# Performance work log

Hardware: AMD Instinct MI355X
Metric: run time of the kernel (lower is better)

## Reference

```python
import jax, jax.numpy as jnp
import numpy as np

B = 1; D = 28; H = 28; W = 28; DIM = 192; HEADS = 6
WS = (7, 7, 7); SS = (3, 3, 3)
CH = DIM // HEADS
N = WS[0] * WS[1] * WS[2]
ND, NH, NWW = D // WS[0], H // WS[1], W // WS[2]
NW = ND * NH * NWW
L = D * H * W
HID = 4 * DIM


def _rel_pos_index():
    c = np.stack(np.meshgrid(np.arange(WS[0]), np.arange(WS[1]), np.arange(WS[2]), indexing='ij')).reshape(3, -1)
    r = (c[:, :, None] - c[:, None, :]).transpose(1, 2, 0)
    r[:, :, 0] += WS[0] - 1; r[:, :, 1] += WS[1] - 1; r[:, :, 2] += WS[2] - 1
    r[:, :, 0] *= (2 * WS[1] - 1) * (2 * WS[2] - 1)
    r[:, :, 1] *= 2 * WS[2] - 1
    return r.sum(-1).reshape(-1)

RPI = _rel_pos_index()  # (N*N,)


def _attn_mask():
    img = np.zeros((D, H, W), np.float32)
    cnt = 0
    sl = lambda w, s: (slice(0, -w), slice(-w, -s), slice(-s, None))
    for a in sl(WS[0], SS[0]):
        for bb in sl(WS[1], SS[1]):
            for cc in sl(WS[2], SS[2]):
                img[a, bb, cc] = cnt; cnt += 1
    mw = img.reshape(ND, WS[0], NH, WS[1], NWW, WS[2]).transpose(0, 2, 4, 1, 3, 5).reshape(-1, N)
    return np.where(mw[:, None, :] != mw[:, :, None], np.float32(-100.0), np.float32(0.0))

MASK = jnp.asarray(_attn_mask())  # (NW, N, N)


def ln(x, g, b):
    mu = x.mean(-1, keepdims=True)
    v = ((x - mu) ** 2).mean(-1, keepdims=True)
    return (x - mu) * jax.lax.rsqrt(v + 1e-5) * g + b


def conv3d(x, w, pad):
    return jax.lax.conv_general_dilated(x, w, (1, 1, 1), [(pad, pad)] * 3,
                                        dimension_numbers=('NCDHW', 'OIDHW', 'NCDHW'))


def bn3d(x, g, b):
    mu = x.mean((0, 2, 3, 4), keepdims=True)
    var = x.var((0, 2, 3, 4), keepdims=True)
    return (x - mu) * jax.lax.rsqrt(var + 1e-5) * g.reshape(1, -1, 1, 1, 1) + b.reshape(1, -1, 1, 1, 1)


def offset_block(x, w1, g1, b1, w2, g2, b2, w3):
    x = jax.nn.relu(bn3d(conv3d(x, w1, 1), g1, b1))
    x = jax.nn.relu(bn3d(conv3d(x, w2, 1), g2, b2))
    return conv3d(x, w3, 0)  # (B, 3*HEADS, D, H, W)


def warp(vol, flow):
    # vol: (B,HEADS,CH,D,H,W), flow: (B,HEADS,3,D,H,W) voxel displacements; trilinear, border-clamped
    gd, gh, gw = jnp.meshgrid(jnp.arange(D, dtype=jnp.float32), jnp.arange(H, dtype=jnp.float32),
                              jnp.arange(W, dtype=jnp.float32), indexing='ij')
    cd = jnp.clip(gd + flow[:, :, 0], 0.0, D - 1)
    chh = jnp.clip(gh + flow[:, :, 1], 0.0, H - 1)
    cw = jnp.clip(gw + flow[:, :, 2], 0.0, W - 1)
    d0 = jnp.floor(cd).astype(jnp.int32); d1 = jnp.minimum(d0 + 1, D - 1)
    h0 = jnp.floor(chh).astype(jnp.int32); h1 = jnp.minimum(h0 + 1, H - 1)
    w0 = jnp.floor(cw).astype(jnp.int32); w1 = jnp.minimum(w0 + 1, W - 1)
    fd = (cd - d0).reshape(B, HEADS, 1, -1)
    fh = (chh - h0).reshape(B, HEADS, 1, -1)
    fw = (cw - w0).reshape(B, HEADS, 1, -1)
    vf = vol.reshape(B, HEADS, CH, -1)
    def gat(di, hi, wi):
        idx = ((di * H + hi) * W + wi).reshape(B, HEADS, 1, -1)
        return jnp.take_along_axis(vf, idx, axis=3)
    out = (gat(d0, h0, w0) * (1 - fd) * (1 - fh) * (1 - fw)
           + gat(d0, h0, w1) * (1 - fd) * (1 - fh) * fw
           + gat(d0, h1, w0) * (1 - fd) * fh * (1 - fw)
           + gat(d0, h1, w1) * (1 - fd) * fh * fw
           + gat(d1, h0, w0) * fd * (1 - fh) * (1 - fw)
           + gat(d1, h0, w1) * fd * (1 - fh) * fw
           + gat(d1, h1, w0) * fd * fh * (1 - fw)
           + gat(d1, h1, w1) * fd * fh * fw)
    return out.reshape(B, HEADS, CH, D, H, W)


def win_part(x):  # (B,D,H,W,C) -> (B*NW, N, C)
    c = x.shape[-1]
    x = x.reshape(B, ND, WS[0], NH, WS[1], NWW, WS[2], c)
    return x.transpose(0, 1, 3, 5, 2, 4, 6, 7).reshape(B * NW, N, c)


def dwin_part(x):  # (B,HEADS,D,H,W,CH) -> (B*NW, N, DIM)
    x = x.reshape(B, HEADS, ND, WS[0], NH, WS[1], NWW, WS[2], CH)
    x = x.transpose(0, 2, 4, 6, 3, 5, 7, 1, 8)
    return x.reshape(B * NW, N, DIM)


def win_rev(x):  # (B*NW, N, DIM) -> (B,D,H,W,DIM)
    x = x.reshape(B, ND, NH, NWW, WS[0], WS[1], WS[2], DIM)
    return x.transpose(0, 1, 4, 2, 5, 3, 6, 7).reshape(B, D, H, W, DIM)


def kv(x, w, b):
    y = (x @ w.T + b).reshape(x.shape[0], N, 2, HEADS, CH).transpose(2, 0, 3, 1, 4)
    return y[0], y[1]


def to_heads(x):
    return x.reshape(x.shape[0], N, HEADS, CH).transpose(0, 2, 1, 3)


def _forward(mov, fix, norm1_g, norm1_b, offm_w1, offm_g1, offm_b1, offm_w2, offm_g2, offm_b2, offm_w3, offf_w1, offf_g1, offf_b1, offf_w2, offf_g2, offf_b2, offf_w3, mq_w, mq_b, mkv_w, mkv_b, fq_w, fq_b, fkv_w, fkv_b, mproj_w, mproj_b, fproj_w, fproj_b, rpb_table, norm2_g, norm2_b, fc1_w, fc1_b, fc2_w, fc2_b):
    m = ln(mov, norm1_g, norm1_b).reshape(B, D, H, W, DIM)
    f = ln(fix, norm1_g, norm1_b).reshape(B, D, H, W, DIM)
    off_m = offset_block(jnp.concatenate([m, f], -1).transpose(0, 4, 1, 2, 3), offm_w1, offm_g1, offm_b1, offm_w2, offm_g2, offm_b2, offm_w3)
    off_f = offset_block(jnp.concatenate([f, m], -1).transpose(0, 4, 1, 2, 3), offf_w1, offf_g1, offf_b1, offf_w2, offf_g2, offf_b2, offf_w3)
    mh = m.transpose(0, 4, 1, 2, 3).reshape(B, HEADS, CH, D, H, W)
    fh = f.transpose(0, 4, 1, 2, 3).reshape(B, HEADS, CH, D, H, W)
    dmov = warp(mh, off_m.reshape(B, HEADS, 3, D, H, W)).transpose(0, 1, 3, 4, 5, 2)  # (B,h,D,H,W,c)
    dfix = warp(fh, off_f.reshape(B, HEADS, 3, D, H, W)).transpose(0, 1, 3, 4, 5, 2)
    sh = (-SS[0], -SS[1], -SS[2])
    mw_ = win_part(jnp.roll(m, sh, (1, 2, 3)))
    fw_ = win_part(jnp.roll(f, sh, (1, 2, 3)))
    dmw = dwin_part(jnp.roll(dmov, sh, (2, 3, 4)))
    dfw = dwin_part(jnp.roll(dfix, sh, (2, 3, 4)))
    B_ = B * NW
    scale = CH ** -0.5
    mK, mV = kv(mw_, mkv_w, mkv_b)
    fK, fV = kv(fw_, fkv_w, fkv_b)
    dmQ = to_heads(dmw @ mq_w.T + mq_b) * scale
    dfQ = to_heads(dfw @ fq_w.T + fq_b) * scale
    rpb = rpb_table[RPI].reshape(N, N, HEADS).transpose(2, 0, 1)  # (HEADS,N,N)
    def attend(q, k, v):
        a = jnp.einsum('bhnc,bhmc->bhnm', q, k) + rpb[None]
        a = (a.reshape(B, NW, HEADS, N, N) + MASK[None, :, None]).reshape(B_, HEADS, N, N)
        a = jax.nn.softmax(a, axis=-1)
        return jnp.einsum('bhnm,bhmc->bhnc', a, v).transpose(0, 2, 1, 3).reshape(B_, N, DIM)
    mo = attend(dfQ, mK, mV) @ mproj_w.T + mproj_b
    fo = attend(dmQ, fK, fV) @ fproj_w.T + fproj_b
    mo = jnp.roll(win_rev(mo), SS, (1, 2, 3)).reshape(B, L, DIM)
    fo = jnp.roll(win_rev(fo), SS, (1, 2, 3)).reshape(B, L, DIM)
    m_out = mov + mo
    f_out = fix + fo
    def mlp(x):
        return jax.nn.gelu(x @ fc1_w.T + fc1_b, approximate=False) @ fc2_w.T + fc2_b
    m_out = m_out + mlp(ln(m_out, norm2_g, norm2_b))
    f_out = f_out + mlp(ln(f_out, norm2_g, norm2_b))
    return jnp.stack([m_out, f_out])  # (2, B, L, DIM)


def setup_inputs():
    key = jax.random.key(0)
    ks = iter(jax.random.split(key, 64))
    nrm = lambda shape, s=0.02: jax.random.normal(next(ks), shape, jnp.float32) * s
    d = {}
    d['mov'] = jax.random.normal(next(ks), (B, L, DIM), jnp.float32)
    d['fix'] = jax.random.normal(next(ks), (B, L, DIM), jnp.float32)
    d['norm1_g'] = jnp.ones((DIM,)); d['norm1_b'] = jnp.zeros((DIM,))
    for p in ('offm', 'offf'):
        d[p + '_w1'] = nrm((DIM, 2 * DIM, 3, 3, 3))
        d[p + '_g1'] = jnp.ones((DIM,)); d[p + '_b1'] = jnp.zeros((DIM,))
        d[p + '_w2'] = nrm((DIM // 2, DIM, 3, 3, 3))
        d[p + '_g2'] = jnp.ones((DIM // 2,)); d[p + '_b2'] = jnp.zeros((DIM // 2,))
        d[p + '_w3'] = nrm((3 * HEADS, DIM // 2, 1, 1, 1))
    for p, o in (('mq_w', DIM), ('mkv_w', 2 * DIM), ('fq_w', DIM), ('fkv_w', 2 * DIM), ('mproj_w', DIM), ('fproj_w', DIM)):
        d[p] = nrm((o, DIM))
    for p, o in (('mq_b', DIM), ('mkv_b', 2 * DIM), ('fq_b', DIM), ('fkv_b', 2 * DIM), ('mproj_b', DIM), ('fproj_b', DIM)):
        d[p] = jnp.zeros((o,))
    d['rpb_table'] = nrm(((2 * WS[0] - 1) * (2 * WS[1] - 1) * (2 * WS[2] - 1), HEADS))
    d['norm2_g'] = jnp.ones((DIM,)); d['norm2_b'] = jnp.zeros((DIM,))
    d['fc1_w'] = nrm((HID, DIM)); d['fc1_b'] = jnp.zeros((HID,))
    d['fc2_w'] = nrm((DIM, HID)); d['fc2_b'] = jnp.zeros((DIM,))
    return d


def reference(mov, fix, norm1_g, norm1_b, offm_w1, offm_g1, offm_b1, offm_w2, offm_g2, offm_b2, offm_w3, offf_w1, offf_g1, offf_b1, offf_w2, offf_g2, offf_b2, offf_w3, mq_w, mq_b, mkv_w, mkv_b, fq_w, fq_b, fkv_w, fkv_b, mproj_w, mproj_b, fproj_w, fproj_b, rpb_table, norm2_g, norm2_b, fc1_w, fc1_b, fc2_w, fc2_b):
    return _forward(mov, fix, norm1_g, norm1_b, offm_w1, offm_g1, offm_b1, offm_w2, offm_g2, offm_b2, offm_w3, offf_w1, offf_g1, offf_b1, offf_w2, offf_g2, offf_b2, offf_w3, mq_w, mq_b, mkv_w, mkv_b, fq_w, fq_b, fkv_w, fkv_b, mproj_w, mproj_b, fproj_w, fproj_b, rpb_table, norm2_g, norm2_b, fc1_w, fc1_b, fc2_w, fc2_b)
```

## Files before the change

kernel.cpp:

```cpp
#include <hip/hip_runtime.h>

#define LTOT 21952
#define NTOK 343

typedef unsigned short u16;
typedef unsigned int   u32;
typedef __attribute__((ext_vector_type(8))) short short8;
typedef __attribute__((ext_vector_type(4))) float float4v;

__device__ __forceinline__ u16 f2b(float f){
  u32 x = __float_as_uint(f);
  u32 r = (x + 0x7fffu + ((x>>16)&1u)) >> 16;
  return (u16)r;
}

__device__ __forceinline__ void dma16(const u16* g, u16* l){
  __builtin_amdgcn_global_load_lds((const __attribute__((address_space(1))) u32*)g,
                                   (__attribute__((address_space(3))) u32*)l,
                                   16, 0, 0);
}

__global__ __launch_bounds__(64) void k_ln(const float* __restrict__ mov, const float* __restrict__ fix,
                                           const float* __restrict__ g, const float* __restrict__ b,
                                           float* __restrict__ om, float* __restrict__ of){
// ... 19 lines not shown
  int row = blockIdx.x;
  const float* src = x + (size_t)row*192;
  float* dst = y + (size_t)row*192;
  int t = threadIdx.x;
  float x0 = src[t], x1 = src[t+64], x2 = src[t+128];
  float s = x0+x1+x2, s2 = x0*x0 + x1*x1 + x2*x2;
  for (int o=32;o;o>>=1){ s += __shfl_xor(s,o); s2 += __shfl_xor(s2,o); }
  float mu = s*(1.f/192.f);
  float var = s2*(1.f/192.f) - mu*mu;
  float rs = rsqrtf(var + 1e-5f);
  dst[t]     = (x0-mu)*rs*g[t]     + b[t];
  dst[t+64]  = (x1-mu)*rs*g[t+64]  + b[t+64];
  dst[t+128] = (x2-mu)*rs*g[t+128] + b[t+128];
}

__global__ void k_prepw1b(const float* __restrict__ src, u16* __restrict__ dst, int swap){
  int idx = blockIdx.x*256 + threadIdx.x;
  if (idx >= 192*10368) return;
  int c8 = idx & 7;
  int t2 = idx >> 3;
  int n  = t2 % 192;
  int sw = t2 / 192;
  int k  = (sw>>2)*32 + (sw&3)*8 + c8;
  int t  = k / 384; int c = k - t*384;
  int cs = c + swap; if (cs >= 384) cs -= 384;
  dst[idx] = f2b(src[((size_t)n*384 + cs)*27 + t]);
}
__global__ void k_prepw2b(const float* __restrict__ src, u16* __restrict__ dst){
  int idx = blockIdx.x*256 + threadIdx.x;
  if (idx >= 96*5184) return;
  int n = idx / 5184; int k = idx - n*5184;
  int t = k / 192; int c = k - t*192;
  dst[idx] = f2b(src[((size_t)n*192 + c)*27 + t]);
}
__global__ void k_prepwb(const float* __restrict__ src, u16* __restrict__ dst, int count){
  int idx = blockIdx.x*256 + threadIdx.x;
  if (idx < count) dst[idx] = f2b(src[idx]);
}

__global__ void k_prepbias(const float* __restrict__ rpt, float* __restrict__ bm){
  int idx = blockIdx.x*256 + threadIdx.x;
  if (idx >= 48*123904) return;
  int th = idx / 123904; int r = idx - th*123904;
  int key = r / 352; int q = r - key*352;
  int type = th / 6; int h = th - type*6;
  float v;
  if (key >= 343 || q >= 343){
    v = -30000.f;
  } else {
    int ki = key/49, kj = (key/7)%7, kk = key%7;
    int qi = q/49,   qj = (q/7)%7,   qk = q%7;
    int ridx = ((qi-ki+6)*13 + (qj-kj+6))*13 + (qk-kk+6);
// ... 8 lines not shown

__global__ __launch_bounds__(192) void k_pad1(const float* __restrict__ m_, const float* __restrict__ f_,
                                              u16* __restrict__ xp){
  int p = blockIdx.x; int t = threadIdx.x;
  int pd = p/900; int r = p - pd*900; int ph = r/30; int pw = r - ph*30;
  int d = pd-1, h = ph-1, w = pw-1;
  u16 vm = 0, vf = 0;
  if ((unsigned)d < 28u && (unsigned)h < 28u && (unsigned)w < 28u){
    size_t l = (size_t)((d*28+h)*28+w)*192 + t;
    vm = f2b(m_[l]); vf = f2b(f_[l]);
  }
  xp[(size_t)p*384 + t] = vm;
  xp[(size_t)p*384 + 192 + t] = vf;
}
__global__ __launch_bounds__(192) void k_pad2(const float* __restrict__ t1,
                                              const float* __restrict__ a1, const float* __restrict__ b1,
                                              u16* __restrict__ xp2){
  int p = blockIdx.x; int t = threadIdx.x;
  int pd = p/900; int r = p - pd*900; int ph = r/30; int pw = r - ph*30;
  int d = pd-1, h = ph-1, w = pw-1;
  u16 v = 0;
  if ((unsigned)d < 28u && (unsigned)h < 28u && (unsigned)w < 28u){
    float xv = t1[(size_t)((d*28+h)*28+w)*192 + t];
    v = f2b(fmaxf(xv*a1[t] + b1[t], 0.f));
  }
  xp2[(size_t)p*192 + t] = v;
}

__global__ __launch_bounds__(256, 4) void k_conv1dma(const u16* __restrict__ xp,
                                                     const u16* __restrict__ wmT,
                                                     const u16* __restrict__ wfT,
                                                     float* __restrict__ outm,
                                                     float* __restrict__ outf){
  __shared__ __align__(16) u16 As[2][64*40];
  __shared__ __align__(16) u16 Bs[2][4*1544];
  int tid = threadIdx.x;
  int b0 = blockIdx.x;
  int xcd = b0 & 7, ii = b0 >> 3;
  int bid = (xcd < 6 ? xcd*86 : 516 + (xcd-6)*85) + ii;
  int half = (bid >= 343) ? 1 : 0;
  int t = bid - half*343;
  const u16* wtb = half ? wfT : wmT;
  float* out = half ? outf : outm;
  int v0 = t*64;
  int sv  = tid>>2;
  int c8u = (tid&3)*8;
  int av = v0 + sv;
  int d = av/784; int rm2 = av - d*784; int hh = rm2/28; int ww = rm2 - hh*28;
  int pbase = (d*30 + hh)*30 + ww;
  int lane = tid&63, wv = tid>>6;
// ... 11 lines not shown
    int tp = s/12, cc = s - tp*12;
    int td = tp/9, tr = tp - td*9, th = tr/3, tw = tr - th*3;
    int toff = td*900 + th*30 + tw;
    a_r = *(const uint4*)(xp + (size_t)(pbase + toff)*384 + cc*32 + c8u);
  };
  auto dmaB = [&](int buf, int s){
    const u16* bsrc = wtb + ((size_t)(s*4 + wv)*192)*8 + (size_t)lane*8;
    #pragma unroll
    for (int j=0;j<3;j++)
      dma16(bsrc + j*512, &Bs[buf][wv*1544 + j*512]);
  };
  auto writeA = [&](int buf){
    *(uint4*)(&As[buf][sv*40 + c8u]) = a_r;
  };

  loadA(0);
  dmaB(0, 0);
  writeA(0);
  __syncthreads();
  for (int s = 0; s < 324; s++){
    if (s+1 < 324){ loadA(s+1); dmaB((s+1)&1, s+1); }
    int buf = s&1;
    short8 aa[4], bb[3];
    #pragma unroll
    for (int mt=0; mt<4; mt++)
      aa[mt] = *(const short8*)(&As[buf][(mt*16 + lm)*40 + lq*8]);
    #pragma unroll
    for (int nt=0; nt<3; nt++)
      bb[nt] = *(const short8*)(&Bs[buf][lq*1544 + (nbase + nt*16 + lm)*8]);
    #pragma unroll
    for (int nt=0; nt<3; nt++)
      #pragma unroll
      for (int mt=0; mt<4; mt++)
        acc[mt][nt] = __builtin_amdgcn_mfma_f32_16x16x32_bf16(aa[mt], bb[nt], acc[mt][nt], 0, 0, 0);
    if (s+1 < 324) writeA((s+1)&1);
    __syncthreads();
  }
  #pragma unroll
  for (int mt=0; mt<4; mt++)
    #pragma unroll
    for (int nt=0; nt<3; nt++)
      #pragma unroll
      for (int r=0; r<4; r++){
        int row = v0 + mt*16 + lq*4 + r;
        int col = nbase + nt*16 + lm;
        out[(size_t)row*192 + col] = acc[mt][nt][r];
      }
}

template<int CIN, int COUT>
__global__ __launch_bounds__(256, 4) void k_convmfma(const u16* __restrict__ xpA,
// ... 80 lines not shown
    if (s+1 < STEPS) write_s((s+1)&1);
    __syncthreads();
  }
  #pragma unroll
  for (int mt=0; mt<2; mt++)
    #pragma unroll
    for (int nt=0; nt<NT; nt++)
      #pragma unroll
      for (int r=0; r<4; r++){
        int row = v0 + mbase + mt*16 + lq*4 + r;
        int col = nbase + nt*16 + lm;
        out[(size_t)row*COUT + col] = acc[mt][nt][r];
      }
}

template<int K, int NF, int GATHER, int ASRC, int EPI>
__global__ __launch_bounds__(256) void k_gemm(const float* __restrict__ Af,
                                              const u16* __restrict__ Ab,
                                              const u16* __restrict__ B,
                                              const float* __restrict__ bias,
                                              const float* __restrict__ resid,
                                              float* __restrict__ outf,
                                              u16* __restrict__ out16,
                                              u16* __restrict__ out16b,
                                              float scale){
  constexpr int STEPS = K/32;
  constexpr int NB = NF/64;
  __shared__ __align__(16) u16 As[2][64*40];
  __shared__ __align__(16) u16 Bs[2][64*40];
  __shared__ int map[64];
  int tid = threadIdx.x;
  int bid = blockIdx.x;
  int mb = bid / NB, nb = bid - mb*NB;
  int v0 = mb*64, ncol0 = nb*64;
  if (tid < 64){
    int r = v0 + tid;
    int src;
    if (GATHER == 0){
      src = r;
    } else if (GATHER == 1){
      int w = r/343; int n = r - w*343;
      int nd = w>>4, nh = (w>>2)&3, nw = w&3;
      int i = n/49; int rr = n - i*49; int j = rr/7; int k2 = rr - j*7;
      int dd = nd*7 + i + 3; if (dd >= 28) dd -= 28;
      int hh = nh*7 + j + 3; if (hh >= 28) hh -= 28;
      int ww = nw*7 + k2 + 3; if (ww >= 28) ww -= 28;
      src = (dd*28 + hh)*28 + ww;
    } else {
      int l = r;
      int d = l/784; int rm = l - d*784; int y = rm/28; int x = rm - y*28;
      int dp = d-3; if (dp<0) dp+=28;
      int yp = y-3; if (yp<0) yp+=28;
      int xq = x-3; if (xq<0) xq+=28;
      int nd = dp/7, i = dp - nd*7;
      int nh = yp/7, j = yp - nh*7;
      int nw = xq/7, k2 = xq - nw*7;
      src = ((nd*4+nh)*4+nw)*NTOK + (i*7+j)*7 + k2;
    }
    map[tid] = src;
  }
  __syncthreads();
  int sv = tid>>2, c8 = (tid&3)*8;
  int arow = map[sv];
  int lane = tid&63, wv = tid>>6;
  int lm = lane&15, lq = lane>>4;
  int mbase = (wv>>1)*32, nbase = (wv&1)*32;

  float4v acc[2][2];
  #pragma unroll
  for (int mt=0; mt<2; mt++)
    #pragma unroll
    for (int nt=0; nt<2; nt++) acc[mt][nt] = (float4v)0.f;

  float4 afr0, afr1; uint4 abr; uint4 bvr;
  auto load_s = [&](int s){
    if (ASRC == 0){
      const float* ap = Af + (size_t)arow*K + s*32 + c8;
      afr0 = *(const float4*)ap;
      afr1 = *(const float4*)(ap+4);
    } else {
      abr = *(const uint4*)(Ab + (size_t)arow*K + s*32 + c8);
    }
    bvr = *(const uint4*)(B + (size_t)(ncol0 + sv)*K + s*32 + c8);
  };
  auto write_s = [&](int buf){
    if (ASRC == 0){
      uint4 pk;
      pk.x = (u32)f2b(afr0.x) | ((u32)f2b(afr0.y)<<16);
      pk.y = (u32)f2b(afr0.z) | ((u32)f2b(afr0.w)<<16);
      pk.z = (u32)f2b(afr1.x) | ((u32)f2b(afr1.y)<<16);
      pk.w = (u32)f2b(afr1.z) | ((u32)f2b(afr1.w)<<16);
      *(uint4*)(&As[buf][sv*40 + c8]) = pk;
    } else {
      *(uint4*)(&As[buf][sv*40 + c8]) = abr;
    }
    *(uint4*)(&Bs[buf][sv*40 + c8]) = bvr;
  };

// ... 8 lines not shown
    for (int mt=0; mt<2; mt++)
      aa[mt] = *(const short8*)(&As[buf][(mbase + mt*16 + lm)*40 + lq*8]);
    #pragma unroll
    for (int nt=0; nt<2; nt++)
      bb[nt] = *(const short8*)(&Bs[buf][(nbase + nt*16 + lm)*40 + lq*8]);
    #pragma unroll
    for (int nt=0; nt<2; nt++)
      #pragma unroll
      for (int mt=0; mt<2; mt++)
        acc[mt][nt] = __builtin_amdgcn_mfma_f32_16x16x32_bf16(aa[mt], bb[nt], acc[mt][nt], 0, 0, 0);
    if (s+1 < STEPS) write_s((s+1)&1);
    __syncthreads();
  }
  float bv[2];
  #pragma unroll
  for (int nt=0; nt<2; nt++) bv[nt] = bias ? bias[ncol0 + nbase + nt*16 + lm] : 0.f;
  #pragma unroll
  for (int mt=0; mt<2; mt++){
    #pragma unroll
    for (int r=0; r<4; r++){
      int row = v0 + mbase + mt*16 + lq*4 + r;
      if (EPI == 0 || EPI == 3){
        int w = row/343; int tok = row - w*343;
        #pragma unroll
        for (int nt=0; nt<2; nt++){
          int col = ncol0 + nbase + nt*16 + lm;
          float val = (acc[mt][nt][r] + bv[nt]) * scale;
          if (EPI == 0){
            int h = col>>5, c = col&31;
            out16[((size_t)(w*6 + h)*343 + tok)*32 + c] = f2b(val);
          } else {
            u16* dst = (col < 192) ? out16 : out16b;
            int cc = (col < 192) ? col : col - 192;
            int h = cc>>5, c = cc&31;
            dst[((size_t)(w*6 + h)*343 + tok)*32 + c] = f2b(val);
          }
        }
      } else if (EPI == 1){
        #pragma unroll
        for (int nt=0; nt<2; nt++){
          int col = ncol0 + nbase + nt*16 + lm;
          size_t o = (size_t)row*NF + col;
          outf[o] = acc[mt][nt][r] + bv[nt] + resid[o];
        }
      } else {
        #pragma unroll
        for (int nt=0; nt<2; nt++){
          int col = ncol0 + nbase + nt*16 + lm;
          float v = acc[mt][nt][r] + bv[nt];
          float gl = 0.5f*v*(1.f + erff(v*0.70710678118f));
          out16[(size_t)row*NF + col] = f2b(gl);
        }
      }
    }
  }
}

__global__ __launch_bounds__(192) void k_bnsum(const float* __restrict__ x, int C,
                                               float* __restrict__ psum){
  int bid = blockIdx.x, t = threadIdx.x;
  int rpi = 192/C;
  int c  = (C==192) ? t : (t % 96);
  int ro = (C==192) ? 0 : (t / 96);
  float s=0.f, s2=0.f;
  int base = bid*343;
  for (int r = ro; r < 343; r += rpi){
    float v = x[(size_t)(base+r)*C + c];
    s += v; s2 += v*v;
  }
  psum[(size_t)bid*384 + t]       = s;
  psum[(size_t)bid*384 + 192 + t] = s2;
}
__global__ void k_bnfin(const float* __restrict__ psum, int C,
                        const float* __restrict__ g, const float* __restrict__ b,
                        float* __restrict__ a_out, float* __restrict__ b_out){
  int c = threadIdx.x;
  if (c >= C) return;
  int slots = 192/C;
  float s=0.f, s2=0.f;
  for (int bb=0; bb<64; bb++)
    for (int k=0; k<slots; k++){
      s  += psum[(size_t)bb*384 + k*C + c];
      s2 += psum[(size_t)bb*384 + 192 + k*C + c];
    }
  float mu = s/(float)LTOT;
  float var = s2/(float)LTOT - mu*mu;
  float rstd = rsqrtf(var + 1e-5f);
  float aa = rstd * g[c];
  a_out[c] = aa;
  b_out[c] = b[c] - mu*aa;
}

__global__ __launch_bounds__(96) void k_flow(const float* __restrict__ t2,
                                             const float* __restrict__ a2, const float* __restrict__ b2,
                                             const float* __restrict__ w3, float* __restrict__ flow){
  __shared__ float xr[96];
  int l = blockIdx.x; int t = threadIdx.x;
  float xv = t2[(size_t)l*96 + t];
  xr[t] = fmaxf(xv*a2[t] + b2[t], 0.f);
  __syncthreads();
  if (t < 18){
    float acc = 0.f;
    for (int c=0;c<96;c++) acc += xr[c]*w3[t*96 + c];
    flow[(size_t)t*LTOT + l] = acc;
  }
}

__global__ __launch_bounds__(192) void k_warp(const float* __restrict__ src,
                                              const float* __restrict__ flow, float* __restrict__ dst){
  int l = blockIdx.x; int tid = threadIdx.x; int hh = tid>>5;
  int d = l/784; int rm = l - d*784; int y = rm/28; int x = rm - y*28;
  float fd = flow[(size_t)(hh*3+0)*LTOT + l];
  float fy = flow[(size_t)(hh*3+1)*LTOT + l];
  float fx = flow[(size_t)(hh*3+2)*LTOT + l];
  float cd = fminf(fmaxf((float)d + fd, 0.f), 27.f);
  float cy = fminf(fmaxf((float)y + fy, 0.f), 27.f);
  float cx = fminf(fmaxf((float)x + fx, 0.f), 27.f);
  int d0 = (int)floorf(cd); int d1 = min(d0+1, 27);
  int y0 = (int)floorf(cy); int y1 = min(y0+1, 27);
  int x0 = (int)floorf(cx); int x1 = min(x0+1, 27);
  float wd = cd - (float)d0, wy = cy - (float)y0, wx = cx - (float)x0;
  #define SMP(di,yi,xi) src[(size_t)(((di)*28+(yi))*28+(xi))*192 + tid]
  float v000 = SMP(d0,y0,x0), v001 = SMP(d0,y0,x1), v010 = SMP(d0,y1,x0), v011 = SMP(d0,y1,x1);
  float v100 = SMP(d1,y0,x0), v101 = SMP(d1,y0,x1), v110 = SMP(d1,y1,x0), v111 = SMP(d1,y1,x1);
  #undef SMP
  float o = v000*(1-wd)*(1-wy)*(1-wx) + v001*(1-wd)*(1-wy)*wx
          + v010*(1-wd)*wy*(1-wx)     + v011*(1-wd)*wy*wx
          + v100*wd*(1-wy)*(1-wx)     + v101*wd*(1-wy)*wx
          + v110*wd*wy*(1-wx)         + v111*wd*wy*wx;
  dst[(size_t)l*192 + tid] = o;
}

__global__ __launch_bounds__(256) void k_attmfma(const u16* __restrict__ Q,
                                                 const u16* __restrict__ K,
                                                 const u16* __restrict__ V,
                                                 const float* __restrict__ bm,
                                                 float* __restrict__ ctx){
  __shared__ __align__(16) u16 Kl[352*40];
  __shared__ __align__(16) u16 Vt[32*360];
  __shared__ __align__(16) u16 Pl[4][2][16*40];
  int bid = blockIdx.x;
  int wh = bid/6, qg = bid - (bid/6)*6;
  int w = wh/6, h = wh - w*6;
  int tid = threadIdx.x;
  int nd = w>>4, nh = (w>>2)&3, nw = w&3;
  int type = ((nd==3)?4:0) | ((nh==3)?2:0) | ((nw==3)?1:0);
  const u16* kb = K + (size_t)wh*10976;
  const u16* vbp = V + (size_t)wh*10976;
  for (int idx=tid; idx<343*4; idx+=256){
    int row = idx>>2, c8 = (idx&3)*8;
    uint4 val = *(const uint4*)(kb + row*32 + c8);
    *(uint4*)(&Kl[row*40 + c8]) = val;
  }
  for (int idx=tid; idx<9*40; idx+=256) Kl[343*40 + idx] = 0;
  for (int idx=tid; idx<343*4; idx+=256){
    int row = idx>>2, c8 = (idx&3)*8;
// ... 40 lines not shown
      #pragma unroll
      for (int r=0; r<4; r++){
        float p = __expf(sc[kt][r] - mx);
        sc[kt][r] = p;
        sm += p;
      }
    }
    sm += __shfl_xor(sm, 16);
    sm += __shfl_xor(sm, 32);
    float inv = 1.f/sm;
    float4v o0 = (float4v)0.f, o1 = (float4v)0.f;
    #pragma unroll
    for (int s=0; s<11; s++){
      u16* pw = &Pl[wv][s&1][0];
      #pragma unroll
      for (int half=0; half<2; half++){
        int kt = 2*s + half;
        uint2 pv2;
        pv2.x = (u32)f2b(sc[kt][0]) | ((u32)f2b(sc[kt][1])<<16);
        pv2.y = (u32)f2b(sc[kt][2]) | ((u32)f2b(sc[kt][3])<<16);
        *(uint2*)(&pw[lm*40 + half*16 + lq*4]) = pv2;
      }
      short8 bp = *(const short8*)(&pw[lm*40 + lq*8]);
      short8 a0 = *(const short8*)(&Vt[lm*360 + s*32 + lq*8]);
      short8 a1 = *(const short8*)(&Vt[(16+lm)*360 + s*32 + lq*8]);
      o0 = __builtin_amdgcn_mfma_f32_16x16x32_bf16(a0, bp, o0, 0, 0, 0);
      o1 = __builtin_amdgcn_mfma_f32_16x16x32_bf16(a1, bp, o1, 0, 0, 0);
    }
    int query = q0 + lm;
    if (query < 343){
      float* ob = ctx + ((size_t)w*NTOK + query)*192 + h*32;
      float4 t0, t1v;
      t0.x = o0[0]*inv; t0.y = o0[1]*inv; t0.z = o0[2]*inv; t0.w = o0[3]*inv;
      t1v.x = o1[0]*inv; t1v.y = o1[1]*inv; t1v.z = o1[2]*inv; t1v.w = o1[3]*inv;
      *(float4*)(ob + lq*4) = t0;
      *(float4*)(ob + 16 + lq*4) = t1v;
// ... 35 lines not shown
  const float* mproj_b = (const float*)d_in[28];
  const float* fproj_b = (const float*)d_in[29];
  const float* rpbt    = (const float*)d_in[30];
  const float* n2g     = (const float*)d_in[31];
  const float* n2b     = (const float*)d_in[32];
  const float* fc1_w   = (const float*)d_in[33];
  const float* fc1_b   = (const float*)d_in[34];
  const float* fc2_w   = (const float*)d_in[35];
  const float* fc2_b   = (const float*)d_in[36];
  float* outp = (float*)d_out;

  float* W = (float*)d_ws;
  const size_t L192 = (size_t)LTOT*192;
  float* m_   = W;
  float* f_   = W + 1*L192;
  float* t1m  = W + 2*L192;
  float* t1f  = W + 3*L192;
  u16* xp     = (u16*)(W + 4*L192);
  u16* xp2m   = xp + (size_t)27000*384;
  u16* xp2f   = (u16*)(W + 6*L192);
  float* sb   = W + 6*L192 + 3000000;
  float* a1m = sb,       *b1m = sb+192;
  float* a1f = sb+384,   *b1f = sb+576;
  float* a2m = sb+768,   *b2m = sb+864;
  float* a2f = sb+960,   *b2f = sb+1056;
  float* psum = sb + 1152;
  float* flowm = W + 6*L192 + 3100000;
  float* flowf = flowm + (size_t)LTOT*18;
  float* t2m  = W + 7*L192;
  float* t2f  = W + 7*L192 + (size_t)LTOT*96;
  u16* wt1m = (u16*)(W + 8*L192);
  u16* wt1f = wt1m + 192*10368;
  u16* wt2m = wt1f + 192*10368;
  u16* wt2f = wt2m + 96*5184;
  float* dmov = W + 4*L192;
  float* dfix = W + 5*L192;
  float* ctxm = dmov; float* ctxf = dfix;
  float* mout = m_;   float* fout = f_;
  u16* QMb = (u16*)(W + 6*L192);
  u16* QFb = (u16*)(W + 7*L192);
  u16* Kmb = (u16*)(W + 2*L192);
  u16* Vmb = (u16*)(W + 3*L192);
  u16* Kfb = (u16*)(W + 8*L192);
  u16* Vfb = (u16*)(W + 9*L192);
  float* bm = W;
  u16* wq_m  = (u16*)(W + 9*L192) + 4214784;
  u16* wq_f  = wq_m  + 36864;
  u16* wkv_m = wq_f  + 36864;
  u16* wkv_f = wkv_m + 73728;
  u16* wpj_m = wkv_f + 73728;
  u16* wpj_f = wpj_m + 36864;
  u16* wfc1  = wpj_f + 36864;
  u16* wfc2  = wfc1  + 147456;
  u16* hs16  = (u16*)(W + 2*L192);
  float* lnbuf = W + 6*L192;

  k_prepw1b<<<(192*10368+255)/256, 256, 0, stream>>>(offm_w1, wt1m, 0);
  k_prepw1b<<<(192*10368+255)/256, 256, 0, stream>>>(offf_w1, wt1f, 192);
  k_prepw2b<<<(96*5184+255)/256, 256, 0, stream>>>(offm_w2, wt2m);
  k_prepw2b<<<(96*5184+255)/256, 256, 0, stream>>>(offf_w2, wt2f);
  k_prepwb<<<144, 256, 0, stream>>>(mq_w,    wq_m,  36864);
  k_prepwb<<<144, 256, 0, stream>>>(fq_w,    wq_f,  36864);
  k_prepwb<<<288, 256, 0, stream>>>(mkv_w,   wkv_m, 73728);
  k_prepwb<<<288, 256, 0, stream>>>(fkv_w,   wkv_f, 73728);
  k_prepwb<<<144, 256, 0, stream>>>(mproj_w, wpj_m, 36864);
  k_prepwb<<<144, 256, 0, stream>>>(fproj_w, wpj_f, 36864);
  k_prepwb<<<576, 256, 0, stream>>>(fc1_w,   wfc1,  147456);
  k_prepwb<<<576, 256, 0, stream>>>(fc2_w,   wfc2,  147456);
  k_ln<<<2*LTOT, 64, 0, stream>>>(mov, fix, n1g, n1b, m_, f_);
  k_pad1<<<27000, 192, 0, stream>>>(m_, f_, xp);
  k_conv1dma<<<686, 256, 0, stream>>>(xp, wt1m, wt1f, t1m, t1f);
  k_bnsum<<<64, 192, 0, stream>>>(t1m, 192, psum);
  k_bnfin<<<1, 192, 0, stream>>>(psum, 192, offm_g1, offm_b1, a1m, b1m);
  k_bnsum<<<64, 192, 0, stream>>>(t1f, 192, psum);
  k_bnfin<<<1, 192, 0, stream>>>(psum, 192, offf_g1, offf_b1, a1f, b1f);
  k_pad2<<<27000, 192, 0, stream>>>(t1m, a1m, b1m, xp2m);
  k_pad2<<<27000, 192, 0, stream>>>(t1f, a1f, b1f, xp2f);
  k_convmfma<192,96><<<686, 256, 0, stream>>>(xp2m, xp2f, wt2m, wt2f, t2m, t2f);
  k_bnsum<<<64, 192, 0, stream>>>(t2m, 96, psum);
  k_bnfin<<<1, 96, 0, stream>>>(psum, 96, offm_g2, offm_b2, a2m, b2m);
  k_bnsum<<<64, 192, 0, stream>>>(t2f, 96, psum);
  k_bnfin<<<1, 96, 0, stream>>>(psum, 96, offf_g2, offf_b2, a2f, b2f);
  k_flow<<<LTOT, 96, 0, stream>>>(t2m, a2m, b2m, offm_w3, flowm);
  k_flow<<<LTOT, 96, 0, stream>>>(t2f, a2f, b2f, offf_w3, flowf);
  k_warp<<<LTOT, 192, 0, stream>>>(m_, flowm, dmov);
  k_warp<<<LTOT, 192, 0, stream>>>(f_, flowf, dfix);
  const float scale = 0.17677669529663687f;
  k_gemm<192,192,1,0,0><<<343*3, 256, 0, stream>>>(dmov, nullptr, wq_m,  mq_b,  nullptr, nullptr, QMb, nullptr, scale);
  k_gemm<192,192,1,0,0><<<343*3, 256, 0, stream>>>(dfix, nullptr, wq_f,  fq_b,  nullptr, nullptr, QFb, nullptr, scale);
  k_gemm<192,384,1,0,3><<<343*6, 256, 0, stream>>>(m_,   nullptr, wkv_m, mkv_b, nullptr, nullptr, Kmb, Vmb, 1.f);
  k_gemm<192,384,1,0,3><<<343*6, 256, 0, stream>>>(f_,   nullptr, wkv_f, fkv_b, nullptr, nullptr, Kfb, Vfb, 1.f);
  k_prepbias<<<(48*123904+255)/256, 256, 0, stream>>>(rpbt, bm);
  k_attmfma<<<2304, 256, 0, stream>>>(QFb, Kmb, Vmb, bm, ctxm);
  k_attmfma<<<2304, 256, 0, stream>>>(QMb, Kfb, Vfb, bm, ctxf);
  k_gemm<192,192,2,0,1><<<343*3, 256, 0, stream>>>(ctxm, nullptr, wpj_m, mproj_b, mov, mout, nullptr, nullptr, 1.f);
  k_gemm<192,192,2,0,1><<<343*3, 256, 0, stream>>>(ctxf, nullptr, wpj_f, fproj_b, fix, fout, nullptr, nullptr, 1.f);
  k_ln1<<<LTOT, 64, 0, stream>>>(mout, n2g, n2b, lnbuf);
  k_gemm<192,768,0,0,2><<<343*12, 256, 0, stream>>>(lnbuf, nullptr, wfc1, fc1_b, nullptr, nullptr, hs16, nullptr, 1.f);
  k_gemm<768,192,0,1,1><<<343*3, 256, 0, stream>>>(nullptr, hs16, wfc2, fc2_b, mout, outp, nullptr, nullptr, 1.f);
  k_ln1<<<LTOT, 64, 0, stream>>>(fout, n2g, n2b, lnbuf);
  k_gemm<192,768,0,0,2><<<343*12, 256, 0, stream>>>(lnbuf, nullptr, wfc1, fc1_b, nullptr, nullptr, hs16, nullptr, 1.f);
  k_gemm<768,192,0,1,1><<<343*3, 256, 0, stream>>>(nullptr, hs16, wfc2, fc2_b, fout, outp + L192, nullptr, nullptr, 1.f);
}
```

Before: 1.435 ms.

## Merge moving/fixed kernel launches into batched kernels and triple-buffer conv1

Combines the paired moving/fixed launches (weight prep, BN stats/finalize, pad2, flow, warp, Q/KV/proj GEMMs, attention, LN2 and MLP) into single launches with doubled grids. Per-half pointers are selected from the block index, and contiguous buffers are relied on for the merged LN/MLP path. Separately, conv1 gets a 3-stage LDS pipeline with explicit waitcnt and raw barriers, which lowers its occupancy hint from 4 to 3. The aim is to cut launch count, fill the GPU better in small kernels, and hide load latency in conv1. The cost is more buffer-layout assumptions, e.g. mout/fout and flow halves must be adjacent.

```diff
diff --git a/kernel.cpp b/kernel.cpp
--- a/kernel.cpp
+++ b/kernel.cpp
@@ -57,28 +57,48 @@
   dst[t+128] = (x2-mu)*rs*g[t+128] + b[t+128];
 }
 
-__global__ void k_prepw1b(const float* __restrict__ src, u16* __restrict__ dst, int swap){
+__global__ void k_prepw1b(const float* __restrict__ sm, const float* __restrict__ sf,
+                          u16* __restrict__ dm, u16* __restrict__ df){
   int idx = blockIdx.x*256 + threadIdx.x;
-  if (idx >= 192*10368) return;
-  int c8 = idx & 7;
-  int t2 = idx >> 3;
+  if (idx >= 2*192*10368) return;
+  int half = idx >= 192*10368;
+  int i = idx - half*192*10368;
+  const float* src = half ? sf : sm;
+  u16* dst = half ? df : dm;
+  int swap = half ? 192 : 0;
+  int c8 = i & 7;
+  int t2 = i >> 3;
   int n  = t2 % 192;
   int sw = t2 / 192;
   int k  = (sw>>2)*32 + (sw&3)*8 + c8;
   int t  = k / 384; int c = k - t*384;
   int cs = c + swap; if (cs >= 384) cs -= 384;
-  dst[idx] = f2b(src[((size_t)n*384 + cs)*27 + t]);
-}
-__global__ void k_prepw2b(const float* __restrict__ src, u16* __restrict__ dst){
+  dst[i] = f2b(src[((size_t)n*384 + cs)*27 + t]);
+}
+__global__ void k_prepw2b(const float* __restrict__ sm, const float* __restrict__ sf,
+                          u16* __restrict__ dm, u16* __restrict__ df){
   int idx = blockIdx.x*256 + threadIdx.x;
-  if (idx >= 96*5184) return;
-  int n = idx / 5184; int k = idx - n*5184;
+  if (idx >= 2*96*5184) return;
+  int half = idx >= 96*5184;
+  int i = idx - half*96*5184;
+  const float* src = half ? sf : sm;
+  u16* dst = half ? df : dm;
+  int n = i / 5184; int k = i - n*5184;
   int t = k / 192; int c = k - t*192;
-  dst[idx] = f2b(src[((size_t)n*192 + c)*27 + t]);
-}
-__global__ void k_prepwb(const float* __restrict__ src, u16* __restrict__ dst, int count){
+  dst[i] = f2b(src[((size_t)n*192 + c)*27 + t]);
+}
+__global__ void k_prepwb8(const float* s0,const float* s1,const float* s2,const float* s3,
+                          const float* s4,const float* s5,const float* s6,const float* s7,
+                          u16* d0,u16* d1,u16* d2,u16* d3,u16* d4,u16* d5,u16* d6,u16* d7){
   int idx = blockIdx.x*256 + threadIdx.x;
-  if (idx < count) dst[idx] = f2b(src[idx]);
+  if      (idx < 36864)  d0[idx]        = f2b(s0[idx]);
+  else if (idx < 73728)  d1[idx-36864]  = f2b(s1[idx-36864]);
+  else if (idx < 147456) d2[idx-73728]  = f2b(s2[idx-73728]);
+  else if (idx < 221184) d3[idx-147456] = f2b(s3[idx-147456]);
+  else if (idx < 258048) d4[idx-221184] = f2b(s4[idx-221184]);
+  else if (idx < 294912) d5[idx-258048] = f2b(s5[idx-258048]);
+  else if (idx < 442368) d6[idx-294912] = f2b(s6[idx-294912]);
+  else if (idx < 589824) d7[idx-442368] = f2b(s7[idx-442368]);
 }
 
 __global__ void k_prepbias(const float* __restrict__ rpt, float* __restrict__ bm){
@@ -117,26 +137,28 @@
   xp[(size_t)p*384 + 192 + t] = vf;
 }
 __global__ __launch_bounds__(192) void k_pad2(const float* __restrict__ t1,
-                                              const float* __restrict__ a1, const float* __restrict__ b1,
+                                              const float* __restrict__ sb_,
                                               u16* __restrict__ xp2){
   int p = blockIdx.x; int t = threadIdx.x;
-  int pd = p/900; int r = p - pd*900; int ph = r/30; int pw = r - ph*30;
+  int half = (p >= 27000); int pl = p - half*27000;
+  const float* a1 = sb_ + half*384; const float* b1 = a1 + 192;
+  int pd = pl/900; int r = pl - pd*900; int ph = r/30; int pw = r - ph*30;
   int d = pd-1, h = ph-1, w = pw-1;
   u16 v = 0;
   if ((unsigned)d < 28u && (unsigned)h < 28u && (unsigned)w < 28u){
-    float xv = t1[(size_t)((d*28+h)*28+w)*192 + t];
+    float xv = t1[((size_t)half*LTOT + (d*28+h)*28+w)*192 + t];
     v = f2b(fmaxf(xv*a1[t] + b1[t], 0.f));
   }
   xp2[(size_t)p*192 + t] = v;
 }
 
-__global__ __launch_bounds__(256, 4) void k_conv1dma(const u16* __restrict__ xp,
+__global__ __launch_bounds__(256, 3) void k_conv1dma(const u16* __restrict__ xp,
                                                      const u16* __restrict__ wmT,
                                                      const u16* __restrict__ wfT,
                                                      float* __restrict__ outm,
                                                      float* __restrict__ outf){
-  __shared__ __align__(16) u16 As[2][64*40];
-  __shared__ __align__(16) u16 Bs[2][4*1544];
+  __shared__ __align__(16) u16 As[3][64*40];
+  __shared__ __align__(16) u16 Bs[3][4*1544];
   int tid = threadIdx.x;
   int b0 = blockIdx.x;
   int xcd = b0 & 7, ii = b0 >> 3;
@@ -178,27 +200,37 @@
     *(uint4*)(&As[buf][sv*40 + c8u]) = a_r;
   };
 
-  loadA(0);
-  dmaB(0, 0);
-  writeA(0);
-  __syncthreads();
+  loadA(0); dmaB(0, 0); writeA(0);
+  loadA(1); dmaB(1, 1); writeA(1);
+  asm volatile("s_waitcnt vmcnt(3) lgkmcnt(0)" ::: "memory");
+  __builtin_amdgcn_sched_barrier(0);
+  __builtin_amdgcn_s_barrier();
+  int cur = 0;
   for (int s = 0; s < 324; s++){
-    if (s+1 < 324){ loadA(s+1); dmaB((s+1)&1, s+1); }
-    int buf = s&1;
+    int pf = cur + 2; if (pf >= 3) pf -= 3;
+    if (s < 322){ loadA(s+2); dmaB(pf, s+2); }
     short8 aa[4], bb[3];
     #pragma unroll
     for (int mt=0; mt<4; mt++)
-      aa[mt] = *(const short8*)(&As[buf][(mt*16 + lm)*40 + lq*8]);
+      aa[mt] = *(const short8*)(&As[cur][(mt*16 + lm)*40 + lq*8]);
     #pragma unroll
     for (int nt=0; nt<3; nt++)
-      bb[nt] = *(const short8*)(&Bs[buf][lq*1544 + (nbase + nt*16 + lm)*8]);
+      bb[nt] = *(const short8*)(&Bs[cur][lq*1544 + (nbase + nt*16 + lm)*8]);
     #pragma unroll
     for (int nt=0; nt<3; nt++)
       #pragma unroll
       for (int mt=0; mt<4; mt++)
         acc[mt][nt] = __builtin_amdgcn_mfma_f32_16x16x32_bf16(aa[mt], bb[nt], acc[mt][nt], 0, 0, 0);
-    if (s+1 < 324) writeA((s+1)&1);
-    __syncthreads();
+    if (s < 322){
+      writeA(pf);
+      asm volatile("s_waitcnt vmcnt(3) lgkmcnt(0)" ::: "memory");
+      __builtin_amdgcn_sched_barrier(0);
+    } else {
+      asm volatile("s_waitcnt vmcnt(0) lgkmcnt(0)" ::: "memory");
+      __builtin_amdgcn_sched_barrier(0);
+    }
+    __builtin_amdgcn_s_barrier();
+    cur++; if (cur >= 3) cur = 0;
   }
   #pragma unroll
   for (int mt=0; mt<4; mt++)
@@ -309,7 +341,7 @@
       }
 }
 
-template<int K, int NF, int GATHER, int ASRC, int EPI>
+template<int K, int NF, int GATHER, int ASRC, int EPI, int MRG>
 __global__ __launch_bounds__(256) void k_gemm(const float* __restrict__ Af,
                                               const u16* __restrict__ Ab,
                                               const u16* __restrict__ B,
@@ -318,7 +350,13 @@
                                               float* __restrict__ outf,
                                               u16* __restrict__ out16,
                                               u16* __restrict__ out16b,
-                                              float scale){
+                                              float scale,
+                                              const u16* __restrict__ B2,
+                                              const float* __restrict__ bias2,
+                                              const float* __restrict__ resid2,
+                                              float* __restrict__ outf2,
+                                              u16* __restrict__ out162,
+                                              u16* __restrict__ out16b2){
   constexpr int STEPS = K/32;
   constexpr int NB = NF/64;
   __shared__ __align__(16) u16 As[2][64*40];
@@ -328,8 +366,16 @@
   int bid = blockIdx.x;
   int mb = bid / NB, nb = bid - mb*NB;
   int v0 = mb*64, ncol0 = nb*64;
+  int half = (MRG && v0 >= LTOT) ? 1 : 0;
+  const u16* Bx = half ? B2 : B;
+  const float* biasx = half ? bias2 : bias;
+  const float* residx = half ? resid2 : resid;
+  float* outfx = half ? outf2 : outf;
+  u16* out16x = half ? out162 : out16;
+  u16* out16bx = half ? out16b2 : out16b;
+  int vloc = v0 - half*LTOT;
   if (tid < 64){
-    int r = v0 + tid;
+    int r = vloc + tid;
     int src;
     if (GATHER == 0){
       src = r;
@@ -352,7 +398,7 @@
       int nw = xq/7, k2 = xq - nw*7;
       src = ((nd*4+nh)*4+nw)*NTOK + (i*7+j)*7 + k2;
     }
-    map[tid] = src;
+    map[tid] = src + half*LTOT;
   }
   __syncthreads();
   int sv = tid>>2, c8 = (tid&3)*8;
@@ -376,7 +422,7 @@
     } else {
       abr = *(const uint4*)(Ab + (size_t)arow*K + s*32 + c8);
     }
-    bvr = *(const uint4*)(B + (size_t)(ncol0 + sv)*K + s*32 + c8);
+    bvr = *(const uint4*)(Bx + (size_t)(ncol0 + sv)*K + s*32 + c8);
   };
   auto write_s = [&](int buf){
     if (ASRC == 0){
@@ -415,23 +461,24 @@
   }
   float bv[2];
   #pragma unroll
-  for (int nt=0; nt<2; nt++) bv[nt] = bias ? bias[ncol0 + nbase + nt*16 + lm] : 0.f;
+  for (int nt=0; nt<2; nt++) bv[nt] = biasx ? biasx[ncol0 + nbase + nt*16 + lm] : 0.f;
   #pragma unroll
   for (int mt=0; mt<2; mt++){
     #pragma unroll
     for (int r=0; r<4; r++){
       int row = v0 + mbase + mt*16 + lq*4 + r;
+      int rowl = row - half*LTOT;
       if (EPI == 0 || EPI == 3){
-        int w = row/343; int tok = row - w*343;
+        int w = rowl/343; int tok = rowl - w*343;
         #pragma unroll
         for (int nt=0; nt<2; nt++){
           int col = ncol0 + nbase + nt*16 + lm;
           float val = (acc[mt][nt][r] + bv[nt]) * scale;
           if (EPI == 0){
             int h = col>>5, c = col&31;
-            out16[((size_t)(w*6 + h)*343 + tok)*32 + c] = f2b(val);
+            out16x[((size_t)(w*6 + h)*343 + tok)*32 + c] = f2b(val);
           } else {
-            u16* dst = (col < 192) ? out16 : out16b;
+            u16* dst = (col < 192) ? out16x : out16bx;
             int cc = (col < 192) ? col : col - 192;
             int h = cc>>5, c = cc&31;
             dst[((size_t)(w*6 + h)*343 + tok)*32 + c] = f2b(val);
@@ -441,8 +488,8 @@
         #pragma unroll
         for (int nt=0; nt<2; nt++){
           int col = ncol0 + nbase + nt*16 + lm;
-          size_t o = (size_t)row*NF + col;
-          outf[o] = acc[mt][nt][r] + bv[nt] + resid[o];
+          size_t o = (size_t)rowl*NF + col;
+          outfx[o] = acc[mt][nt][r] + bv[nt] + residx[o];
         }
       } else {
         #pragma unroll
@@ -472,48 +519,62 @@
   psum[(size_t)bid*384 + t]       = s;
   psum[(size_t)bid*384 + 192 + t] = s2;
 }
-__global__ void k_bnfin(const float* __restrict__ psum, int C,
-                        const float* __restrict__ g, const float* __restrict__ b,
-                        float* __restrict__ a_out, float* __restrict__ b_out){
+__global__ void k_bnfin2(const float* __restrict__ psum, int C,
+                         const float* __restrict__ g0, const float* __restrict__ bb0,
+                         const float* __restrict__ g1, const float* __restrict__ bb1,
+                         float* a0, float* b0o, float* a1, float* b1o){
+  int h = blockIdx.x;
   int c = threadIdx.x;
   if (c >= C) return;
+  const float* g  = h ? g1 : g0;
+  const float* bb = h ? bb1 : bb0;
+  float* ao = h ? a1 : a0;
+  float* bo = h ? b1o : b0o;
+  const float* ps = psum + (size_t)h*64*384;
   int slots = 192/C;
   float s=0.f, s2=0.f;
-  for (int bb=0; bb<64; bb++)
+  for (int b=0; b<64; b++)
     for (int k=0; k<slots; k++){
-      s  += psum[(size_t)bb*384 + k*C + c];
-      s2 += psum[(size_t)bb*384 + 192 + k*C + c];
+      s  += ps[(size_t)b*384 + k*C + c];
+      s2 += ps[(size_t)b*384 + 192 + k*C + c];
     }
   float mu = s/(float)LTOT;
   float var = s2/(float)LTOT - mu*mu;
   float rstd = rsqrtf(var + 1e-5f);
   float aa = rstd * g[c];
-  a_out[c] = aa;
-  b_out[c] = b[c] - mu*aa;
+  ao[c] = aa;
+  bo[c] = bb[c] - mu*aa;
 }
 
 __global__ __launch_bounds__(96) void k_flow(const float* __restrict__ t2,
-                                             const float* __restrict__ a2, const float* __restrict__ b2,
-                                             const float* __restrict__ w3, float* __restrict__ flow){
+                                             const float* __restrict__ a2b,
+                                             const float* __restrict__ w3m,
+                                             const float* __restrict__ w3f,
+                                             float* __restrict__ flow){
   __shared__ float xr[96];
   int l = blockIdx.x; int t = threadIdx.x;
+  int half = l >= LTOT; int ll = l - half*LTOT;
+  const float* a2 = a2b + half*192; const float* b2 = a2 + 96;
+  const float* w3 = half ? w3f : w3m;
   float xv = t2[(size_t)l*96 + t];
   xr[t] = fmaxf(xv*a2[t] + b2[t], 0.f);
   __syncthreads();
   if (t < 18){
     float acc = 0.f;
     for (int c=0;c<96;c++) acc += xr[c]*w3[t*96 + c];
-    flow[(size_t)t*LTOT + l] = acc;
+    flow[((size_t)half*18 + t)*LTOT + ll] = acc;
   }
 }
 
 __global__ __launch_bounds__(192) void k_warp(const float* __restrict__ src,
                                               const float* __restrict__ flow, float* __restrict__ dst){
   int l = blockIdx.x; int tid = threadIdx.x; int hh = tid>>5;
-  int d = l/784; int rm = l - d*784; int y = rm/28; int x = rm - y*28;
-  float fd = flow[(size_t)(hh*3+0)*LTOT + l];
-  float fy = flow[(size_t)(hh*3+1)*LTOT + l];
-  float fx = flow[(size_t)(hh*3+2)*LTOT + l];
+  int half = l >= LTOT; int ll = l - half*LTOT;
+  const float* s_ = src + (size_t)half*LTOT*192;
+  int d = ll/784; int rm = ll - d*784; int y = rm/28; int x = rm - y*28;
+  float fd = flow[((size_t)half*18 + hh*3+0)*LTOT + ll];
+  float fy = flow[((size_t)half*18 + hh*3+1)*LTOT + ll];
+  float fx = flow[((size_t)half*18 + hh*3+2)*LTOT + ll];
   float cd = fminf(fmaxf((float)d + fd, 0.f), 27.f);
   float cy = fminf(fmaxf((float)y + fy, 0.f), 27.f);
   float cx = fminf(fmaxf((float)x + fx, 0.f), 27.f);
@@ -521,7 +582,7 @@
   int y0 = (int)floorf(cy); int y1 = min(y0+1, 27);
   int x0 = (int)floorf(cx); int x1 = min(x0+1, 27);
   float wd = cd - (float)d0, wy = cy - (float)y0, wx = cx - (float)x0;
-  #define SMP(di,yi,xi) src[(size_t)(((di)*28+(yi))*28+(xi))*192 + tid]
+  #define SMP(di,yi,xi) s_[(size_t)(((di)*28+(yi))*28+(xi))*192 + tid]
   float v000 = SMP(d0,y0,x0), v001 = SMP(d0,y0,x1), v010 = SMP(d0,y1,x0), v011 = SMP(d0,y1,x1);
   float v100 = SMP(d1,y0,x0), v101 = SMP(d1,y0,x1), v110 = SMP(d1,y1,x0), v111 = SMP(d1,y1,x1);
   #undef SMP
@@ -532,15 +593,25 @@
   dst[(size_t)l*192 + tid] = o;
 }
 
-__global__ __launch_bounds__(256) void k_attmfma(const u16* __restrict__ Q,
-                                                 const u16* __restrict__ K,
-                                                 const u16* __restrict__ V,
+__global__ __launch_bounds__(256) void k_attmfma(const u16* __restrict__ Q1,
+                                                 const u16* __restrict__ K1,
+                                                 const u16* __restrict__ V1,
+                                                 const u16* __restrict__ Q2,
+                                                 const u16* __restrict__ K2,
+                                                 const u16* __restrict__ V2,
                                                  const float* __restrict__ bm,
-                                                 float* __restrict__ ctx){
+                                                 float* __restrict__ ctx1,
+                                                 float* __restrict__ ctx2){
   __shared__ __align__(16) u16 Kl[352*40];
   __shared__ __align__(16) u16 Vt[32*360];
   __shared__ __align__(16) u16 Pl[4][2][16*40];
-  int bid = blockIdx.x;
+  int bid0 = blockIdx.x;
+  int halfsel = bid0 >= 2304;
+  int bid = bid0 - halfsel*2304;
+  const u16* Q = halfsel ? Q2 : Q1;
+  const u16* K = halfsel ? K2 : K1;
+  const u16* V = halfsel ? V2 : V1;
+  float* ctx = halfsel ? ctx2 : ctx1;
   int wh = bid/6, qg = bid - (bid/6)*6;
   int w = wh/6, h = wh - w*6;
   int tid = threadIdx.x;
@@ -611,12 +682,12 @@
     for (int s=0; s<11; s++){
       u16* pw = &Pl[wv][s&1][0];
       #pragma unroll
-      for (int half=0; half<2; half++){
-        int kt = 2*s + half;
+      for (int hf=0; hf<2; hf++){
+        int kt = 2*s + hf;
         uint2 pv2;
         pv2.x = (u32)f2b(sc[kt][0]) | ((u32)f2b(sc[kt][1])<<16);
         pv2.y = (u32)f2b(sc[kt][2]) | ((u32)f2b(sc[kt][3])<<16);
-        *(uint2*)(&pw[lm*40 + half*16 + lq*4]) = pv2;
+        *(uint2*)(&pw[lm*40 + hf*16 + lq*4]) = pv2;
       }
       short8 bp = *(const short8*)(&pw[lm*40 + lq*8]);
       short8 a0 = *(const short8*)(&Vt[lm*360 + s*32 + lq*8]);
@@ -682,21 +753,17 @@
   const size_t L192 = (size_t)LTOT*192;
   float* m_   = W;
   float* f_   = W + 1*L192;
-  float* t1m  = W + 2*L192;
-  float* t1f  = W + 3*L192;
+  float* t1   = W + 2*L192;
   u16* xp     = (u16*)(W + 4*L192);
-  u16* xp2m   = xp + (size_t)27000*384;
-  u16* xp2f   = (u16*)(W + 6*L192);
+  u16* xp2    = xp + (size_t)27000*384;
   float* sb   = W + 6*L192 + 3000000;
   float* a1m = sb,       *b1m = sb+192;
   float* a1f = sb+384,   *b1f = sb+576;
   float* a2m = sb+768,   *b2m = sb+864;
   float* a2f = sb+960,   *b2f = sb+1056;
-  float* psum = sb + 1152;
+  float* psum = sb + 1536;
   float* flowm = W + 6*L192 + 3100000;
-  float* flowf = flowm + (size_t)LTOT*18;
-  float* t2m  = W + 7*L192;
-  float* t2f  = W + 7*L192 + (size_t)LTOT*96;
+  float* t2   = W + 7*L192;
   u16* wt1m = (u16*)(W + 8*L192);
   u16* wt1f = wt1m + 192*10368;
   u16* wt2m = wt1f + 192*10368;
@@ -723,50 +790,34 @@
   u16* hs16  = (u16*)(W + 2*L192);
   float* lnbuf = W + 6*L192;
 
-  k_prepw1b<<<(192*10368+255)/256, 256, 0, stream>>>(offm_w1, wt1m, 0);
-  k_prepw1b<<<(192*10368+255)/256, 256, 0, stream>>>(offf_w1, wt1f, 192);
-  k_prepw2b<<<(96*5184+255)/256, 256, 0, stream>>>(offm_w2, wt2m);
-  k_prepw2b<<<(96*5184+255)/256, 256, 0, stream>>>(offf_w2, wt2f);
-  k_prepwb<<<144, 256, 0, stream>>>(mq_w,    wq_m,  36864);
-  k_prepwb<<<144, 256, 0, stream>>>(fq_w,    wq_f,  36864);
-  k_prepwb<<<288, 256, 0, stream>>>(mkv_w,   wkv_m, 73728);
-  k_prepwb<<<288, 256, 0, stream>>>(fkv_w,   wkv_f, 73728);
-  k_prepwb<<<144, 256, 0, stream>>>(mproj_w, wpj_m, 36864);
-  k_prepwb<<<144, 256, 0, stream>>>(fproj_w, wpj_f, 36864);
-  k_prepwb<<<576, 256, 0, stream>>>(fc1_w,   wfc1,  147456);
-  k_prepwb<<<576, 256, 0, stream>>>(fc2_w,   wfc2,  147456);
+  k_prepw1b<<<(2*192*10368+255)/256, 256, 0, stream>>>(offm_w1, offf_w1, wt1m, wt1f);
+  k_prepw2b<<<(2*96*5184+255)/256, 256, 0, stream>>>(offm_w2, offf_w2, wt2m, wt2f);
+  k_prepwb8<<<2304, 256, 0, stream>>>(mq_w, fq_w, mkv_w, fkv_w, mproj_w, fproj_w, fc1_w, fc2_w,
+                                      wq_m, wq_f, wkv_m, wkv_f, wpj_m, wpj_f, wfc1, wfc2);
   k_ln<<<2*LTOT, 64, 0, stream>>>(mov, fix, n1g, n1b, m_, f_);
   k_pad1<<<27000, 192, 0, stream>>>(m_, f_, xp);
-  k_conv1dma<<<686, 256, 0, stream>>>(xp, wt1m, wt1f, t1m, t1f);
-  k_bnsum<<<64, 192, 0, stream>>>(t1m, 192, psum);
-  k_bnfin<<<1, 192, 0, stream>>>(psum, 192, offm_g1, offm_b1, a1m, b1m);
-  k_bnsum<<<64, 192, 0, stream>>>(t1f, 192, psum);
-  k_bnfin<<<1, 192, 0, stream>>>(psum, 192, offf_g1, offf_b1, a1f, b1f);
-  k_pad2<<<27000, 192, 0, stream>>>(t1m, a1m, b1m, xp2m);
-  k_pad2<<<27000, 192, 0, stream>>>(t1f, a1f, b1f, xp2f);
-  k_convmfma<192,96><<<686, 256, 0, stream>>>(xp2m, xp2f, wt2m, wt2f, t2m, t2f);
-  k_bnsum<<<64, 192, 0, stream>>>(t2m, 96, psum);
-  k_bnfin<<<1, 96, 0, stream>>>(psum, 96, offm_g2, offm_b2, a2m, b2m);
-  k_bnsum<<<64, 192, 0, stream>>>(t2f, 96, psum);
-  k_bnfin<<<1, 96, 0, stream>>>(psum, 96, offf_g2, offf_b2, a2f, b2f);
-  k_flow<<<LTOT, 96, 0, stream>>>(t2m, a2m, b2m, offm_w3, flowm);
-  k_flow<<<LTOT, 96, 0, stream>>>(t2f, a2f, b2f, offf_w3, flowf);
-  k_warp<<<LTOT, 192, 0, stream>>>(m_, flowm, dmov);
-  k_warp<<<LTOT, 192, 0, stream>>>(f_, flowf, dfix);
+  k_conv1dma<<<686, 256, 0, stream>>>(xp, wt1m, wt1f, t1, t1 + 2*L192);
+  k_bnsum<<<128, 192, 0, stream>>>(t1, 192, psum);
+  k_bnfin2<<<2, 192, 0, stream>>>(psum, 192, offm_g1, offm_b1, offf_g1, offf_b1, a1m, b1m, a1f, b1f);
+  k_pad2<<<54000, 192, 0, stream>>>(t1, sb, xp2);
+  k_convmfma<192,96><<<686, 256, 0, stream>>>(xp2, xp2 + (size_t)27000*192, wt2m, wt2f,
+                                              t2, t2 + (size_t)LTOT*96);
+  k_bnsum<<<128, 192, 0, stream>>>(t2, 96, psum);
+  k_bnfin2<<<2, 96, 0, stream>>>(psum, 96, offm_g2, offm_b2, offf_g2, offf_b2, a2m, b2m, a2f, b2f);
+  k_flow<<<2*LTOT, 96, 0, stream>>>(t2, sb+768, offm_w3, offf_w3, flowm);
+  k_warp<<<2*LTOT, 192, 0, stream>>>(m_, flowm, dmov);
   const float scale = 0.17677669529663687f;
-  k_gemm<192,192,1,0,0><<<343*3, 256, 0, stream>>>(dmov, nullptr, wq_m,  mq_b,  nullptr, nullptr, QMb, nullptr, scale);
-  k_gemm<192,192,1,0,0><<<343*3, 256, 0, stream>>>(dfix, nullptr, wq_f,  fq_b,  nullptr, nullptr, QFb, nullptr, scale);
-  k_gemm<192,384,1,0,3><<<343*6, 256, 0, stream>>>(m_,   nullptr, wkv_m, mkv_b, nullptr, nullptr, Kmb, Vmb, 1.f);
-  k_gemm<192,384,1,0,3><<<343*6, 256, 0, stream>>>(f_,   nullptr, wkv_f, fkv_b, nullptr, nullptr, Kfb, Vfb, 1.f);
+  k_gemm<192,192,1,0,0,1><<<2*343*3, 256, 0, stream>>>(dmov, nullptr, wq_m, mq_b, nullptr, nullptr, QMb, nullptr, scale,
+                                                       wq_f, fq_b, nullptr, nullptr, QFb, nullptr);
+  k_gemm<192,384,1,0,3,1><<<2*343*6, 256, 0, stream>>>(m_, nullptr, wkv_m, mkv_b, nullptr, nullptr, Kmb, Vmb, 1.f,
+                                                       wkv_f, fkv_b, nullptr, nullptr, Kfb, Vfb);
   k_prepbias<<<(48*123904+255)/256, 256, 0, stream>>>(rpbt, bm);
-  k_attmfma<<<2304, 256, 0, stream>>>(QFb, Kmb, Vmb, bm, ctxm);
-  k_attmfma<<<2304, 256, 0, stream>>>(QMb, Kfb, Vfb, bm, ctxf);
-  k_gemm<192,192,2,0,1><<<343*3, 256, 0, stream>>>(ctxm, nullptr, wpj_m, mproj_b, mov, mout, nullptr, nullptr, 1.f);
-  k_gemm<192,192,2,0,1><<<343*3, 256, 0, stream>>>(ctxf, nullptr, wpj_f, fproj_b, fix, fout, nullptr, nullptr, 1.f);
-  k_ln1<<<LTOT, 64, 0, stream>>>(mout, n2g, n2b, lnbuf);
-  k_gemm<192,768,0,0,2><<<343*12, 256, 0, stream>>>(lnbuf, nullptr, wfc1, fc1_b, nullptr, nullptr, hs16, nullptr, 1.f);
-  k_gemm<768,192,0,1,1><<<343*3, 256, 0, stream>>>(nullptr, hs16, wfc2, fc2_b, mout, outp, nullptr, nullptr, 1.f);
-  k_ln1<<<LTOT, 64, 0, stream>>>(fout, n2g, n2b, lnbuf);
-  k_gemm<192,768,0,0,2><<<343*12, 256, 0, stream>>>(lnbuf, nullptr, wfc1, fc1_b, nullptr, nullptr, hs16, nullptr, 1.f);
-  k_gemm<768,192,0,1,1><<<343*3, 256, 0, stream>>>(nullptr, hs16, wfc2, fc2_b, fout, outp + L192, nullptr, nullptr, 1.f);
-}
+  k_attmfma<<<4608, 256, 0, stream>>>(QFb, Kmb, Vmb, QMb, Kfb, Vfb, bm, ctxm, ctxf);
+  k_gemm<192,192,2,0,1,1><<<2*343*3, 256, 0, stream>>>(ctxm, nullptr, wpj_m, mproj_b, mov, mout, nullptr, nullptr, 1.f,
+                                                       wpj_f, fproj_b, fix, fout, nullptr, nullptr);
+  k_ln1<<<2*LTOT, 64, 0, stream>>>(mout, n2g, n2b, lnbuf);
+  k_gemm<192,768,0,0,2,0><<<2*343*12, 256, 0, stream>>>(lnbuf, nullptr, wfc1, fc1_b, nullptr, nullptr, hs16, nullptr, 1.f,
+                                                        nullptr, nullptr, nullptr, nullptr, nullptr, nullptr);
+  k_gemm<768,192,0,1,1,0><<<2*343*3, 256, 0, stream>>>(nullptr, hs16, wfc2, fc2_b, mout, outp, nullptr, nullptr, 1.f,
+                                                       nullptr, nullptr, nullptr, nullptr, nullptr, nullptr);
+}
```

Measured after the change: 1.210 ms (median of 2 runs). 1.19x faster.
